# Kernel tuning notes

Hardware: AMD Instinct MI355X
Metric: run time of the kernel (lower is better)

## Reference

```python
import jax, jax.numpy as jnp
import numpy as np

B, S, D_IN = 16, 2048, 8
H = 512
WIN = 10
D = D_IN + 1  # time-augmented path dim
SIG_DIM = D + D * D + D * D * D  # depth-3 signature channels = 819


def setup_inputs() -> dict:
    key = jax.random.key(0)
    ks = jax.random.split(key, 5)
    s = 1.0 / np.sqrt(H)
    return {
        "x": jax.random.normal(ks[0], (B, S, D_IN), jnp.float32),
        "W_ih": jax.random.uniform(ks[1], (4 * H, D_IN + SIG_DIM), jnp.float32, -s, s),
        "W_hh": jax.random.uniform(ks[2], (4 * H, H), jnp.float32, -s, s),
        "b_ih": jax.random.uniform(ks[3], (4 * H,), jnp.float32, -s, s),
        "b_hh": jax.random.uniform(ks[4], (4 * H,), jnp.float32, -s, s),
    }


def _windowed_signatures(x):
    # x: (B, S, D_IN). Returns per-step depth-3 signatures of the trailing
    # window of the time-augmented path, with a zero basepoint prepended.
    b, s, _ = x.shape
    time = jnp.linspace(0.0, 1.0, s, dtype=x.dtype)
    xt = jnp.concatenate(
        [x, jnp.broadcast_to(time[None, :, None], (b, s, 1))], axis=-1
    )  # (B,S,D)
    # Window indices clipped at 0: repeated points give zero increments, which
    # leave the signature unchanged (exp(0)=Id). This exactly reproduces the
    # short-window and t=0 duplicated-path cases of the torch module.
    idx = jnp.clip(
        jnp.arange(s)[:, None] - (WIN - 1) + jnp.arange(WIN)[None, :], 0, s - 1
    )
    win = xt[:, idx, :]
    # Zero basepoint -> first increment is the first window point itself.
    incs = jnp.concatenate([win[:, :, :1, :], jnp.diff(win, axis=2)], axis=2)
    incs = jnp.moveaxis(incs, 2, 0)

    def chen_step(carry, dx):
        # Chen's identity: S <- S (tensor) exp(dx), truncated at depth 3.
        s1, s2, s3 = carry
        e2 = 0.5 * dx[..., :, None] * dx[..., None, :]
        e3 = (dx[..., :, None, None] * dx[..., None, :, None] * dx[..., None, None, :]) / 6.0
        n3 = (s3
              + s2[..., :, :, None] * dx[..., None, None, :]
              + s1[..., :, None, None] * e2[..., None, :, :]
              + e3)
        n2 = s2 + s1[..., :, None] * dx[..., None, :] + e2
        n1 = s1 + dx
        return (n1, n2, n3), None

    z1 = jnp.zeros((b, s, D), x.dtype)
    z2 = jnp.zeros((b, s, D, D), x.dtype)
    z3 = jnp.zeros((b, s, D, D, D), x.dtype)
    (s1, s2, s3), _ = jax.lax.scan(chen_step, (z1, z2, z3), incs)
    return jnp.concatenate(
        [s1, s2.reshape(b, s, D * D), s3.reshape(b, s, D * D * D)], axis=-1
    )  # (B, S, SIG_DIM), level-major lexicographic order as in signatory


def reference(x, W_ih, W_hh, b_ih, b_hh):
    b = x.shape[0]
    sigs = _windowed_signatures(x)
    x_aug = jnp.concatenate([x, sigs], axis=-1)  # (B, S, D_IN + SIG_DIM)
    bias = b_ih + b_hh

    def lstm_step(carry, xt):
        h, c = carry
        g = xt @ W_ih.T + h @ W_hh.T + bias
        i, f, gg, o = jnp.split(g, 4, axis=-1)  # torch gate order i,f,g,o
        c = jax.nn.sigmoid(f) * c + jax.nn.sigmoid(i) * jnp.tanh(gg)
        h = jax.nn.sigmoid(o) * jnp.tanh(c)
        return (h, c), h

    h0 = jnp.zeros((b, H), x.dtype)
    (hn, cn), ys = jax.lax.scan(lstm_step, (h0, h0), jnp.swapaxes(x_aug, 0, 1))
    return jnp.swapaxes(ys, 0, 1), hn, cn
```

## Files before the change

### kernel.cpp

```cpp
#include <hip/hip_runtime.h>
#include <hip/hip_bf16.h>
#include <stdint.h>

typedef short bf16x8 __attribute__((ext_vector_type(8)));
typedef float f32x4 __attribute__((ext_vector_type(4)));

#define B_ 16
#define S_ 2048
#define H_ 512
#define NG 2048
#define KA 827
#define KP 832
#define NPOS (B_*S_)

#define OFF_XAUG 0
#define OFF_WIHB 54525952
#define OFF_G    57933824
#define OFF_RING 0
#define RING_U64_PER_SLOT 2048
#define SENT32 0x7F807F80u
#define SENT64 0x7F807F807F807F80ull

__device__ __forceinline__ unsigned short f2bf(float f){
  union { float f; unsigned u; } v; v.f = f;
  unsigned u = v.u;
  unsigned r = (u + 0x7FFFu + ((u >> 16) & 1u)) >> 16;
  return (unsigned short)r;
}
__device__ __forceinline__ float bf2f(unsigned short s){
  union { unsigned u; float f; } v; v.u = ((unsigned)s) << 16;
  return v.f;
}
__device__ __forceinline__ float sigf(float x){ return 1.0f / (1.0f + __expf(-x)); }
__device__ __forceinline__ float tanhfast(float x){ return 1.0f - 2.0f / (__expf(2.0f*x) + 1.0f); }

__global__ __launch_bounds__(256) void sigk(const float* __restrict__ x,
                                            unsigned short* __restrict__ xaug){
  const int bid = blockIdx.x;
  const int s = bid >> 4, b = bid & 15;
  const int tid = threadIdx.x;
  __shared__ float win[10][9];
  __shared__ float s1b[2][9];
  __shared__ float s2b[2][81];
  if (tid < 90){
    int w = tid / 9, d = tid - w*9;
    int idx = s - 9 + w; if (idx < 0) idx = 0;
    win[w][d] = (d < 8) ? x[((size_t)b*S_ + idx)*8 + d] : (float)idx * (1.0f/2047.0f);
  }
  if (tid < 81) s2b[0][tid] = 0.0f;
  if (tid < 9)  s1b[0][tid] = 0.0f;
  __syncthreads();
  const int i0 = tid / 81;
  const int jj = (tid / 9) % 9;
  const int kk = tid % 9;
  float r0 = 0.0f, r1 = 0.0f, r2 = 0.0f;
  int p = 0;
  for (int w = 0; w < 10; ++w){
    if (tid < 243){
      float dj  = win[w][jj]   - (w ? win[w-1][jj]   : 0.0f);
      float dk  = win[w][kk]   - (w ? win[w-1][kk]   : 0.0f);
      float di0 = win[w][i0]   - (w ? win[w-1][i0]   : 0.0f);
      float di1 = win[w][i0+3] - (w ? win[w-1][i0+3] : 0.0f);
      float di2 = win[w][i0+6] - (w ? win[w-1][i0+6] : 0.0f);
      float e2 = 0.5f * dj * dk;
      float e3 = dj * dk * (1.0f/6.0f);
      r0 += s2b[p][i0*9+jj]*dk     + s1b[p][i0]*e2   + di0*e3;
      r1 += s2b[p][(i0+3)*9+jj]*dk + s1b[p][i0+3]*e2 + di1*e3;
      r2 += s2b[p][(i0+6)*9+jj]*dk + s1b[p][i0+6]*e2 + di2*e3;
    }
    if (tid < 81){
      int si = tid / 9, sj = tid - si*9;
      float dsi = win[w][si] - (w ? win[w-1][si] : 0.0f);
      float dsj = win[w][sj] - (w ? win[w-1][sj] : 0.0f);
      s2b[p^1][tid] = s2b[p][tid] + s1b[p][si]*dsj + 0.5f*dsi*dsj;
    }
    if (tid < 9){
      float dt = win[w][tid] - (w ? win[w-1][tid] : 0.0f);
      s1b[p^1][tid] = s1b[p][tid] + dt;
    }
    __syncthreads();
    p ^= 1;
  }
  unsigned short* row = xaug + (size_t)bid * KP;
  if (tid < 8)  row[tid]      = f2bf(x[((size_t)b*S_ + s)*8 + tid]);
  if (tid < 9)  row[8 + tid]  = f2bf(s1b[p][tid]);
  if (tid < 81) row[17 + tid] = f2bf(s2b[p][tid]);
  if (tid < 243){
    row[98 + tid]       = f2bf(r0);
    row[98 + tid + 243] = f2bf(r1);
    row[98 + tid + 486] = f2bf(r2);
  }
  if (tid < KP - KA) row[KA + tid] = 0;
}

__global__ void convk(const float* __restrict__ W, unsigned short* __restrict__ o){
  int idx = blockIdx.x*256 + threadIdx.x;
  if (idx >= NG*KP) return;
  int n = idx / KP, k = idx - n*KP;
  o[idx] = (k < KA) ? f2bf(W[(size_t)n*KA + k]) : (unsigned short)0;
}

__global__ __launch_bounds__(256) void gemmk(const unsigned short* __restrict__ A,
                                             const unsigned short* __restrict__ Bw,
                                             unsigned short* __restrict__ G){
  __shared__ unsigned short as[128][40];
  __shared__ unsigned short bs[128][40];
  const int tid = threadIdx.x;
  const int l = tid & 63, w = tid >> 6;
  const int wr = w >> 1, wc = w & 1;
  const int M0 = blockIdx.x * 128, N0 = blockIdx.y * 128;
  f32x4 acc[4][4];
  for (int i=0;i<4;i++) for (int j2=0;j2<4;j2++) acc[i][j2] = (f32x4){0,0,0,0};
  const int lrow = l & 15, kq8 = (l >> 4) * 8;
  for (int kt = 0; kt < 26; ++kt){
    const int kbase = kt * 32;
    for (int c = tid; c < 512; c += 256){
      int row = c >> 2, kc = (c & 3) * 8;
      uint4 va = *(const uint4*)(A  + (size_t)(M0 + row)*KP + kbase + kc);
      *(uint4*)(&as[row][kc]) = va;
      uint4 vb = *(const uint4*)(Bw + (size_t)(N0 + row)*KP + kbase + kc);
      *(uint4*)(&bs[row][kc]) = vb;
    }
    __syncthreads();
    bf16x8 af[4], bfv[4];
    for (int i=0;i<4;i++)    af[i]  = *(const bf16x8*)(&as[wr*64 + i*16 + lrow][kq8]);
    for (int j2=0;j2<4;j2++) bfv[j2] = *(const bf16x8*)(&bs[wc*64 + j2*16 + lrow][kq8]);
    for (int i=0;i<4;i++)
      for (int j2=0;j2<4;j2++)
        acc[i][j2] = __builtin_amdgcn_mfma_f32_16x16x32_bf16(af[i], bfv[j2], acc[i][j2], 0, 0, 0);
    __syncthreads();
  }
  const int rq = (l >> 4) * 4;
  for (int i=0;i<4;i++){
    for (int q=0;q<4;q++){
      int grow_ = M0 + wr*64 + i*16 + rq + q;
      unsigned short* gout = G + (size_t)grow_*NG + N0 + wc*64 + lrow;
      for (int j2=0;j2<4;j2++)
        gout[j2*16] = f2bf(acc[i][j2][q]);
    }
  }
}

__global__ __launch_bounds__(256) void sentk(uint4* __restrict__ ring){
  const size_t i = (size_t)blockIdx.x*256 + threadIdx.x;
  uint4 s; s.x = SENT32; s.y = SENT32; s.z = SENT32; s.w = SENT32;
  #pragma unroll
  for (int k = 0; k < 8; ++k)
    ring[i + (size_t)k*262144] = s;
}

__global__ __launch_bounds__(64, 1) void recurk(const float* __restrict__ Whh,
    const float* __restrict__ bih, const float* __restrict__ bhh,
    const unsigned short* __restrict__ G, float* __restrict__ out,
    unsigned long long* __restrict__ ring){
  const int W = ((blockIdx.x & 7) << 3) | (blockIdx.x >> 3);
  const int l = threadIdx.x;
  const int b = l & 15, kq = l >> 4;
  const int hbase = W * 8;

  bf16x8 a0[16], a1[16];
  {
    const int p = l & 15;
    const int arow0 = (p < 8) ? (hbase + p) : (512 + hbase + (p - 8));
    const int arow1 = arow0 + 1024;
    const float* w0 = Whh + (size_t)arow0 * H_;
    const float* w1 = Whh + (size_t)arow1 * H_;
    for (int kk2 = 0; kk2 < 16; ++kk2){
      const int k0 = kk2*32 + kq*8;
      float4 v0 = *(const float4*)(w0 + k0);
      float4 v1 = *(const float4*)(w0 + k0 + 4);
      bf16x8 av;
      av[0]=(short)f2bf(v0.x); av[1]=(short)f2bf(v0.y); av[2]=(short)f2bf(v0.z); av[3]=(short)f2bf(v0.w);
      av[4]=(short)f2bf(v1.x); av[5]=(short)f2bf(v1.y); av[6]=(short)f2bf(v1.z); av[7]=(short)f2bf(v1.w);
      a0[kk2] = av;
      float4 u0 = *(const float4*)(w1 + k0);
      float4 u1 = *(const float4*)(w1 + k0 + 4);
      bf16x8 bv2;
      bv2[0]=(short)f2bf(u0.x); bv2[1]=(short)f2bf(u0.y); bv2[2]=(short)f2bf(u0.z); bv2[3]=(short)f2bf(u0.w);
      bv2[4]=(short)f2bf(u1.x); bv2[5]=(short)f2bf(u1.y); bv2[6]=(short)f2bf(u1.z); bv2[7]=(short)f2bf(u1.w);
      a1[kk2] = bv2;
    }
  }
  const int col0 = ((kq < 2) ? (kq*4) : (512 + (kq-2)*4)) + hbase;
  const int col1 = col0 + 1024;
  float bias0[4], bias1[4];
  #pragma unroll
  for (int q=0;q<4;q++){
    bias0[q] = bih[col0+q] + bhh[col0+q];
    bias1[q] = bih[col1+q] + bhh[col1+q];
  }
  const bool low = (kq < 2);
  const int hcol = hbase + (low ? kq*4 : (kq-2)*4);
  const size_t ownw = (size_t)W*32 + b*2 + kq;
  float cr[4] = {0,0,0,0};

  for (int t = 0; t < S_; ++t){
    const unsigned short* gp = G + ((size_t)t*16 + b) * NG;
    const short4 g0 = *(const short4*)(gp + col0);
    const short4 g1 = *(const short4*)(gp + col1);

    f32x4 acc0 = (f32x4){0,0,0,0}, acc0b = (f32x4){0,0,0,0};
    f32x4 acc1 = (f32x4){0,0,0,0}, acc1b = (f32x4){0,0,0,0};
    if (t){
      const unsigned long long* sp = ring + (size_t)(t-1)*RING_U64_PER_SLOT;
      unsigned long long rv[32];
      for (;;){
        #pragma unroll
        for (int i = 0; i < 16; ++i){
          const size_t wi = (size_t)((i*4 + kq)*32 + b*2);
          rv[2*i]   = __hip_atomic_load(sp + wi,     __ATOMIC_RELAXED, __HIP_MEMORY_SCOPE_AGENT);
          rv[2*i+1] = __hip_atomic_load(sp + wi + 1, __ATOMIC_RELAXED, __HIP_MEMORY_SCOPE_AGENT);
        }
        unsigned ok = 1;
        #pragma unroll
        for (int i = 0; i < 32; ++i) ok &= (rv[i] != SENT64);
        if (__all((int)ok)) break;
      }
      #pragma unroll
      for (int i = 0; i < 8; ++i){
        uint2 lo0 = __builtin_bit_cast(uint2, rv[4*i]);
        uint2 hi0 = __builtin_bit_cast(uint2, rv[4*i+1]);
        uint4 u0v; u0v.x = lo0.x; u0v.y = lo0.y; u0v.z = hi0.x; u0v.w = hi0.y;
        bf16x8 bv0 = __builtin_bit_cast(bf16x8, u0v);
        acc0  = __builtin_amdgcn_mfma_f32_16x16x32_bf16(a0[2*i],   bv0, acc0,  0, 0, 0);
        acc1  = __builtin_amdgcn_mfma_f32_16x16x32_bf16(a1[2*i],   bv0, acc1,  0, 0, 0);
        uint2 lo1 = __builtin_bit_cast(uint2, rv[4*i+2]);
        uint2 hi1 = __builtin_bit_cast(uint2, rv[4*i+3]);
        uint4 u1v; u1v.x = lo1.x; u1v.y = lo1.y; u1v.z = hi1.x; u1v.w = hi1.y;
        bf16x8 bv1 = __builtin_bit_cast(bf16x8, u1v);
        acc0b = __builtin_amdgcn_mfma_f32_16x16x32_bf16(a0[2*i+1], bv1, acc0b, 0, 0, 0);
        acc1b = __builtin_amdgcn_mfma_f32_16x16x32_bf16(a1[2*i+1], bv1, acc1b, 0, 0, 0);
      }
    }
    float ga0[4] = { bf2f((unsigned short)g0.x), bf2f((unsigned short)g0.y),
                     bf2f((unsigned short)g0.z), bf2f((unsigned short)g0.w) };
    float ga1[4] = { bf2f((unsigned short)g1.x), bf2f((unsigned short)g1.y),
                     bf2f((unsigned short)g1.z), bf2f((unsigned short)g1.w) };
    float own0[4], own1[4], oth0[4], oth1[4];
    #pragma unroll
    for (int q=0;q<4;q++){
      own0[q] = (acc0[q] + acc0b[q]) + ga0[q] + bias0[q];
      own1[q] = (acc1[q] + acc1b[q]) + ga1[q] + bias1[q];
    }
    #pragma unroll
    for (int q=0;q<4;q++){
      oth0[q] = __shfl_xor(own0[q], 32, 64);
      oth1[q] = __shfl_xor(own1[q], 32, 64);
    }
    float h4[4];
    #pragma unroll
    for (int q=0;q<4;q++){
      float iv = low ? own0[q] : oth0[q];
      float fv = low ? oth0[q] : own0[q];
      float gv = low ? own1[q] : oth1[q];
      float ov = low ? oth1[q] : own1[q];
      cr[q] = sigf(fv)*cr[q] + sigf(iv)*tanhfast(gv);
      h4[q] = sigf(ov)*tanhfast(cr[q]);
    }
    if (low){
      unsigned long long pk = (unsigned long long)f2bf(h4[0])
                            | ((unsigned long long)f2bf(h4[1]) << 16)
                            | ((unsigned long long)f2bf(h4[2]) << 32)
                            | ((unsigned long long)f2bf(h4[3]) << 48);
      __hip_atomic_exchange(ring + (size_t)t*RING_U64_PER_SLOT + ownw,
                            pk, __ATOMIC_RELAXED, __HIP_MEMORY_SCOPE_AGENT);
      if (t == S_ - 1){
        float* hn = out + (size_t)B_*S_*H_;
        float* cn = hn + B_*H_;
        #pragma unroll
        for (int q=0;q<4;q++){
          hn[b*H_ + hcol + q] = h4[q];
          cn[b*H_ + hcol + q] = cr[q];
        }
      }
    }
  }
}

__global__ __launch_bounds__(256) void outk(const unsigned long long* __restrict__ ring,
                                            float* __restrict__ out){
  const size_t idx = (size_t)blockIdx.x*256 + threadIdx.x;
  const int w = (int)(idx & 127);
  const size_t bt = idx >> 7;
  const int t = (int)(bt & 2047);
  const int b = (int)(bt >> 11);
  const int hcol = w * 4;
  const int W = hcol >> 3;
  const int kq = (hcol >> 2) & 1;
  unsigned long long v = ring[(size_t)t*RING_U64_PER_SLOT + (size_t)W*32 + b*2 + kq];
  float4 o;
  o.x = bf2f((unsigned short)(v));
  o.y = bf2f((unsigned short)(v >> 16));
  o.z = bf2f((unsigned short)(v >> 32));
  o.w = bf2f((unsigned short)(v >> 48));
  *(float4*)(out + ((size_t)b*S_ + t)*H_ + hcol) = o;
}

extern "C" void kernel_launch(void* const* d_in, const int* in_sizes, int n_in,
                              void* d_out, int out_size, void* d_ws, size_t ws_size,
                              hipStream_t stream){
  const float* x   = (const float*)d_in[0];
  const float* Wih = (const float*)d_in[1];
  const float* Whh = (const float*)d_in[2];
  const float* bih = (const float*)d_in[3];
  const float* bhh = (const float*)d_in[4];
  float* out = (float*)d_out;
  char* ws = (char*)d_ws;
  unsigned short* xaug     = (unsigned short*)(ws + OFF_XAUG);
  unsigned short* wihb     = (unsigned short*)(ws + OFF_WIHB);
  unsigned short* G        = (unsigned short*)(ws + OFF_G);
  unsigned long long* ring = (unsigned long long*)(ws + OFF_RING);

  sigk<<<NPOS, 256, 0, stream>>>(x, xaug);
  convk<<<(NG*KP + 255)/256, 256, 0, stream>>>(Wih, wihb);
  gemmk<<<dim3(256, 16), 256, 0, stream>>>(xaug, wihb, G);
  sentk<<<1024, 256, 0, stream>>>((uint4*)(ws + OFF_RING));
  recurk<<<64, 64, 0, stream>>>(Whh, bih, bhh, G, out, ring);
  outk<<<16384, 256, 0, stream>>>(ring, out);
}
```

Baseline: 4.911 ms.

## Pack four recurrence waves per block and share h via LDS

The persistent recurrence kernel now runs 16 blocks of 256 threads instead of 64 single-wave blocks. Each block cooperatively polls the global ring slot with coalesced loads, agrees on readiness through shared flags and __syncthreads, stages the hidden state in LDS, and each wave then reads its MFMA operands from LDS. This cuts redundant global polling traffic per step, since each wave previously loaded the whole slot itself. In exchange it adds two or three block-wide barriers per timestep, and four waves now share a CU rather than each having one to itself.

```diff
diff --git a/kernel.cpp b/kernel.cpp
--- a/kernel.cpp
+++ b/kernel.cpp
@@ -149,12 +149,16 @@
     ring[i + (size_t)k*262144] = s;
 }
 
-__global__ __launch_bounds__(64, 1) void recurk(const float* __restrict__ Whh,
+__global__ __launch_bounds__(256, 1) void recurk(const float* __restrict__ Whh,
     const float* __restrict__ bih, const float* __restrict__ bhh,
     const unsigned short* __restrict__ G, float* __restrict__ out,
     unsigned long long* __restrict__ ring){
-  const int W = ((blockIdx.x & 7) << 3) | (blockIdx.x >> 3);
-  const int l = threadIdx.x;
+  __shared__ unsigned long long hbuf[RING_U64_PER_SLOT];
+  __shared__ int wflag[4];
+  const int tid = threadIdx.x;
+  const int wid = tid >> 6;
+  const int l = tid & 63;
+  const int W = (int)blockIdx.x * 4 + wid;
   const int b = l & 15, kq = l >> 4;
   const int hbase = W * 8;
 
@@ -203,31 +207,34 @@
     f32x4 acc1 = (f32x4){0,0,0,0}, acc1b = (f32x4){0,0,0,0};
     if (t){
       const unsigned long long* sp = ring + (size_t)(t-1)*RING_U64_PER_SLOT;
-      unsigned long long rv[32];
+      unsigned long long rv[8];
       for (;;){
         #pragma unroll
-        for (int i = 0; i < 16; ++i){
-          const size_t wi = (size_t)((i*4 + kq)*32 + b*2);
-          rv[2*i]   = __hip_atomic_load(sp + wi,     __ATOMIC_RELAXED, __HIP_MEMORY_SCOPE_AGENT);
-          rv[2*i+1] = __hip_atomic_load(sp + wi + 1, __ATOMIC_RELAXED, __HIP_MEMORY_SCOPE_AGENT);
-        }
+        for (int j = 0; j < 8; ++j)
+          rv[j] = __hip_atomic_load(sp + tid + j*256, __ATOMIC_RELAXED, __HIP_MEMORY_SCOPE_AGENT);
         unsigned ok = 1;
         #pragma unroll
-        for (int i = 0; i < 32; ++i) ok &= (rv[i] != SENT64);
-        if (__all((int)ok)) break;
+        for (int j = 0; j < 8; ++j) ok &= (rv[j] != SENT64);
+        const int wok = __all((int)ok);
+        if (l == 0) wflag[wid] = wok;
+        __syncthreads();
+        const int allok = wflag[0] & wflag[1] & wflag[2] & wflag[3];
+        __syncthreads();
+        if (allok) break;
       }
       #pragma unroll
+      for (int j = 0; j < 8; ++j) hbuf[tid + j*256] = rv[j];
+      __syncthreads();
+      uint4 hv[16];
+      #pragma unroll
+      for (int i = 0; i < 16; ++i)
+        hv[i] = *(const uint4*)&hbuf[(i*4 + kq)*32 + b*2];
+      #pragma unroll
       for (int i = 0; i < 8; ++i){
-        uint2 lo0 = __builtin_bit_cast(uint2, rv[4*i]);
-        uint2 hi0 = __builtin_bit_cast(uint2, rv[4*i+1]);
-        uint4 u0v; u0v.x = lo0.x; u0v.y = lo0.y; u0v.z = hi0.x; u0v.w = hi0.y;
-        bf16x8 bv0 = __builtin_bit_cast(bf16x8, u0v);
+        bf16x8 bv0 = __builtin_bit_cast(bf16x8, hv[2*i]);
         acc0  = __builtin_amdgcn_mfma_f32_16x16x32_bf16(a0[2*i],   bv0, acc0,  0, 0, 0);
         acc1  = __builtin_amdgcn_mfma_f32_16x16x32_bf16(a1[2*i],   bv0, acc1,  0, 0, 0);
-        uint2 lo1 = __builtin_bit_cast(uint2, rv[4*i+2]);
-        uint2 hi1 = __builtin_bit_cast(uint2, rv[4*i+3]);
-        uint4 u1v; u1v.x = lo1.x; u1v.y = lo1.y; u1v.z = hi1.x; u1v.w = hi1.y;
-        bf16x8 bv1 = __builtin_bit_cast(bf16x8, u1v);
+        bf16x8 bv1 = __builtin_bit_cast(bf16x8, hv[2*i+1]);
         acc0b = __builtin_amdgcn_mfma_f32_16x16x32_bf16(a0[2*i+1], bv1, acc0b, 0, 0, 0);
         acc1b = __builtin_amdgcn_mfma_f32_16x16x32_bf16(a1[2*i+1], bv1, acc1b, 0, 0, 0);
       }
@@ -315,6 +322,6 @@
   convk<<<(NG*KP + 255)/256, 256, 0, stream>>>(Wih, wihb);
   gemmk<<<dim3(256, 16), 256, 0, stream>>>(xaug, wihb, G);
   sentk<<<1024, 256, 0, stream>>>((uint4*)(ws + OFF_RING));
-  recurk<<<64, 64, 0, stream>>>(Whh, bih, bhh, G, out, ring);
+  recurk<<<16, 256, 0, stream>>>(Whh, bih, bhh, G, out, ring);
   outk<<<16384, 256, 0, stream>>>(ring, out);
 }
```

Measured after the change: 5.855 ms. 1.19x slower.
